# Performance work log

Measured on AMD Instinct MI355X. Metric: run time of the kernel, lower is better.

The kernel has to match this reference:

```python
import jax, jax.numpy as jnp
import numpy as np

B, L, NUM_AA, E, H = 128, 2048, 20, 16, 128

def _mlp(x, W1, b1, W2, b2, W3, b3):
    h = jax.nn.relu(x @ W1 + b1)
    h = jax.nn.relu(h @ W2 + b2)
    return h @ W3 + b3

def _mlp_params(key, in_dim):
    k1, k2, k3 = jax.random.split(key, 3)
    W1 = jax.random.normal(k1, (in_dim, H), jnp.float32) / np.sqrt(in_dim)
    W2 = jax.random.normal(k2, (H, H), jnp.float32) / np.sqrt(H)
    W3 = jax.random.normal(k3, (H, 1), jnp.float32) / np.sqrt(H)
    return W1, jnp.zeros((H,), jnp.float32), W2, jnp.zeros((H,), jnp.float32), W3, jnp.zeros((1,), jnp.float32)

def setup_inputs() -> dict:
    key = jax.random.key(0)
    kR, ks, ke, kl, kt, kp = jax.random.split(key, 6)
    inp = {
        'R': jax.random.normal(kR, (B, L, 3), jnp.float32) * 3.8,  # ~CA-CA scale
        'seq': jax.random.randint(ks, (B, L), 0, NUM_AA),
        'emb': jax.random.normal(ke, (NUM_AA, E), jnp.float32),
    }
    for pref, k, d in (('fl', kl, 1 + 2 * E), ('ft', kt, 1 + 3 * E), ('fp', kp, 2 + 4 * E)):
        W1, b1, W2, b2, W3, b3 = _mlp_params(k, d)
        inp.update({f'{pref}_W1': W1, f'{pref}_b1': b1, f'{pref}_W2': W2, f'{pref}_b2': b2, f'{pref}_W3': W3, f'{pref}_b3': b3})
    return inp

def _energy(R, e, fl, ft, fp):
    d = R[:, 1:, :] - R[:, :-1, :]                      # [B,L-1,3] bond vectors
    lengths = jnp.linalg.norm(d, axis=-1)               # [B,L-1]
    x_l = jnp.concatenate([lengths[..., None], e[:, :-1, :], e[:, 1:, :]], axis=-1)
    E_l = _mlp(x_l, *fl)[..., 0].sum(axis=1)
    # bond angles at atom i+1 between (R[i]-R[i+1]) and (R[i+2]-R[i+1])
    u, v = -d[:, :-1, :], d[:, 1:, :]                   # [B,L-2,3]
    cos_t = jnp.sum(u * v, axis=-1) / (jnp.linalg.norm(u, axis=-1) * jnp.linalg.norm(v, axis=-1))
    theta_in = jnp.clip(cos_t, -1.0, 1.0)               # use_cos_theta=True -> cos(arccos(clip))
    x_t = jnp.concatenate([theta_in[..., None], e[:, :-2, :], e[:, 1:-1, :], e[:, 2:, :]], axis=-1)
    E_t = _mlp(x_t, *ft)[..., 0].sum(axis=1)
    # torsions over quadruples
    b1, b2, b3 = d[:, :-2, :], d[:, 1:-1, :], d[:, 2:, :]
    n1 = jnp.cross(b1, b2)
    n2 = jnp.cross(b2, b3)
    b2u = b2 / jnp.linalg.norm(b2, axis=-1, keepdims=True)
    m1 = jnp.cross(n1, b2u)
    phi = jnp.arctan2(jnp.sum(m1 * n2, axis=-1), jnp.sum(n1 * n2, axis=-1))  # [B,L-3]
    sc = jnp.stack([jnp.sin(phi), jnp.cos(phi)], axis=-1)                    # [B,L-3,2]
    x_p = jnp.concatenate([sc, e[:, :-3, :], e[:, 1:-2, :], e[:, 2:-1, :], e[:, 3:, :]], axis=-1)
    E_p = _mlp(x_p, *fp)[..., 0].sum(axis=1)
    return E_l + E_t + E_p

def reference(R, seq, emb,
              fl_W1, fl_b1, fl_W2, fl_b2, fl_W3, fl_b3,
              ft_W1, ft_b1, ft_W2, ft_b2, ft_W3, ft_b3,
              fp_W1, fp_b1, fp_W2, fp_b2, fp_W3, fp_b3):
    e = emb[seq]                                        # [B,L,E]
    return _energy(R, e,
                   (fl_W1, fl_b1, fl_W2, fl_b2, fl_W3, fl_b3),
                   (ft_W1, ft_b1, ft_W2, ft_b2, ft_W3, ft_b3),
                   (fp_W1, fp_b1, fp_W2, fp_b2, fp_W3, fp_b3))
```

## Files before the change

kernel.cpp:

```cpp
#include <hip/hip_runtime.h>


typedef short bf16x8  __attribute__((ext_vector_type(8)));
typedef float f32x4   __attribute__((ext_vector_type(4)));
typedef float f32x16  __attribute__((ext_vector_type(16)));

constexpr int Lc  = 2048;
constexpr int SHs = 136;

union FragU { uint4 u; bf16x8 v; };

__device__ __forceinline__ unsigned short f2bf(float f) {
    union { float f; unsigned u; } v; v.f = f;
    unsigned u = v.u;
    u = u + 0x7FFFu + ((u >> 16) & 1u);
    return (unsigned short)(u >> 16);
}

__device__ __forceinline__ unsigned pkbf(float a, float b) {
    unsigned ua = __float_as_uint(a) + 0x8000u;
    unsigned ub = __float_as_uint(b) + 0x8000u;
    return __builtin_amdgcn_perm(ub, ua, 0x07060302u);
}

__global__ __launch_bounds__(256)
void prep_kernel(const float* __restrict__ W1_0, const float* __restrict__ b1_0,
                 const float* __restrict__ W1_1, const float* __restrict__ b1_1,
                 const float* __restrict__ W1_2, const float* __restrict__ b1_2,
                 const float* __restrict__ W2_0, const float* __restrict__ W2_1,
                 const float* __restrict__ W2_2,
                 const float* __restrict__ emb, char* __restrict__ ws,
                 float* __restrict__ out)
{
    const int tid = blockIdx.x * 256 + threadIdx.x;
    const int np  = gridDim.x * 256;
    if (blockIdx.x == 0 && threadIdx.x < 128) out[threadIdx.x] = 0.0f;

    unsigned short* d2 = (unsigned short*)ws;
    for (int o = tid; o < 3 * 16384; o += np) {
        int t = o >> 14, r = o & 16383, col = r >> 7, k = r & 127;
        const float* W2 = (t == 0) ? W2_0 : (t == 1) ? W2_1 : W2_2;
        d2[o] = f2bf(W2[k * 128 + col]);
    }
    unsigned short* d1 = (unsigned short*)(ws + 98304);
    for (int o = tid; o < 3 * 12288; o += np) {
        int t = o / 12288, r = o - t * 12288, hid = r / 96, k = r - hid * 96;
        const int NE16 = (t == 0) ? 32 : (t == 1) ? 48 : 64;
        const int NG   = (t == 2) ? 2 : 1;
        const float* W1 = (t == 0) ? W1_0 : (t == 1) ? W1_1 : W1_2;
        const float* b1 = (t == 0) ? b1_0 : (t == 1) ? b1_1 : b1_2;
        float v = 0.0f;
        if (k >= 16) {
            int j = k - 16;
            if (j < NE16) v = W1[(NG + j) * 128 + hid];
        } else if (k == 4) v = b1[hid];
        else if (t == 0 && k == 0) v = W1_0[hid];
        else if (t == 1 && k == 1) v = W1_1[hid];
        else if (t == 2 && k == 2) v = W1_2[hid];
        else if (t == 2 && k == 3) v = W1_2[128 + hid];
        d1[o] = f2bf(v);
    }
    unsigned short* eb = (unsigned short*)(ws + 172032);
    for (int i = tid; i < 320; i += np) eb[i] = f2bf(emb[i]);
}

struct SMem {
    unsigned short H1s[128 * SHs];
    float  Rbuf[393];
    uint2  geomh[128];
    int    seqb[132];
    unsigned short ebuf[320];
    float  part[4];
};

template<int TYPE>
__device__ __forceinline__ void type_pass(
    SMem& sm, const char* __restrict__ ws,
    const float* __restrict__ b2, const float* __restrict__ w3,
    int i0, int wv, int ln31, int hi, f32x4& p4)
{
    constexpr int NEMB  = (TYPE == 0) ? 2 : (TYPE == 1) ? 3 : 4;
    constexpr int STEPS = 1 + NEMB;
    constexpr int ROWSB = Lc - 1 - TYPE;

    const unsigned short* w1t = (const unsigned short*)(ws + 98304 + TYPE * 24576);
    const unsigned short* w2t = (const unsigned short*)(ws + TYPE * 32768);
    const f32x4 z4 = (f32x4){0.f, 0.f, 0.f, 0.f};

    FragU A1[STEPS];
#pragma unroll
    for (int s = 0; s < STEPS; ++s)
        A1[s].u = *(const uint4*)&w1t[(wv * 32 + ln31) * 96 + s * 16 + hi * 8];

#pragma unroll
    for (int h = 0; h < 2; ++h) {
        f32x16 acc1[2];
        acc1[0] = (f32x16)(0.f);
        acc1[1] = (f32x16)(0.f);

#pragma unroll
        for (int s = 0; s < STEPS; ++s) {
#pragma unroll
            for (int rt = 0; rt < 2; ++rt) {
                const int row = h * 64 + rt * 32 + ln31;
                FragU bb;
                if (s == 0) {
                    if (hi == 0) {
                        uint2 g = sm.geomh[row];
                        bb.u = make_uint4(g.x, g.y, 0x00003F80u, 0u);
                    } else {
                        bb.u = make_uint4(0u, 0u, 0u, 0u);
                    }
                } else {
                    bb.u = *(const uint4*)&sm.ebuf[sm.seqb[row + (s - 1)] * 16 + hi * 8];
                }
                acc1[rt] = __builtin_amdgcn_mfma_f32_32x32x16_bf16(A1[s].v, bb.v, acc1[rt], 0, 0, 0);
            }
        }

#pragma unroll
        for (int rt = 0; rt < 2; ++rt) {
            const int row = h * 64 + rt * 32 + ln31;
#pragma unroll
            for (int g = 0; g < 4; ++g) {
                float v0 = fmaxf(acc1[rt][4 * g + 0], 0.f);
                float v1 = fmaxf(acc1[rt][4 * g + 1], 0.f);
                float v2 = fmaxf(acc1[rt][4 * g + 2], 0.f);
                float v3 = fmaxf(acc1[rt][4 * g + 3], 0.f);
                uint2 pk;
                pk.x = pkbf(v0, v1);
                pk.y = pkbf(v2, v3);
                *(uint2*)&sm.H1s[row * SHs + wv * 32 + 8 * g + 4 * hi] = pk;
            }
        }
    }

    FragU B2[8];
#pragma unroll
    for (int s2 = 0; s2 < 8; ++s2)
        B2[s2].u = *(const uint4*)&w2t[(wv * 32 + ln31) * 128 + s2 * 16 + hi * 8];
    const float b2v = b2[wv * 32 + ln31];
    const float w3v = w3[wv * 32 + ln31];
    __syncthreads();

#pragma unroll
    for (int h = 0; h < 2; ++h) {
        f32x16 acc2[2];
        acc2[0] = (f32x16)(0.f);
        acc2[1] = (f32x16)(0.f);
#pragma unroll
        for (int s2 = 0; s2 < 8; ++s2)
#pragma unroll
            for (int rt = 0; rt < 2; ++rt) {
                const int row = h * 64 + rt * 32 + ln31;
                bf16x8 aa = *(const bf16x8*)&sm.H1s[row * SHs + s2 * 16 + hi * 8];
                acc2[rt] = __builtin_amdgcn_mfma_f32_32x32x16_bf16(aa, B2[s2].v, acc2[rt], 0, 0, 0);
            }

#pragma unroll
        for (int rt = 0; rt < 2; ++rt) {
#pragma unroll
            for (int g = 0; g < 4; ++g) {
                const int rbase = i0 + h * 64 + rt * 32 + 8 * g + 4 * hi;
                f32x4 v;
                v[0] = acc2[rt][4 * g + 0]; v[1] = acc2[rt][4 * g + 1];
                v[2] = acc2[rt][4 * g + 2]; v[3] = acc2[rt][4 * g + 3];
                v = __builtin_elementwise_max(v + b2v, z4);
                if (rbase + 3 < ROWSB) {
                    p4 += v * w3v;
                } else {
#pragma unroll
                    for (int rg = 0; rg < 4; ++rg)
                        if (rbase + rg < ROWSB) p4[rg] += v[rg] * w3v;
                }
            }
        }
    }
    __syncthreads();
}

__global__ __launch_bounds__(256, 4)
void energy_kernel(const float* __restrict__ R, const int* __restrict__ seq,
                   const char* __restrict__ ws,
                   const float* b2_0, const float* b2_1, const float* b2_2,
                   const float* w3_0, const float* w3_1, const float* w3_2,
                   const float* b3_0, const float* b3_1, const float* b3_2,
                   float* __restrict__ out)
{
    __shared__ SMem sm;
    const int tid = threadIdx.x;
    const int b   = blockIdx.y;
    const int i0  = blockIdx.x * 128;
    const int lane = tid & 63, wv = tid >> 6;
    const int ln31 = lane & 31, hi = lane >> 5;

    for (int t = tid; t < 393; t += 256) {
        int lr = t / 3, comp = t - lr * 3;
        int row = min(i0 + lr, Lc - 1);
        sm.Rbuf[t] = R[((size_t)b * Lc + row) * 3 + comp];
    }
    for (int t = tid; t < 131; t += 256)
        sm.seqb[t] = seq[b * Lc + min(i0 + t, Lc - 1)];
    {
        const uint4* se = (const uint4*)(ws + 172032);
        for (int t = tid; t < 40; t += 256) ((uint4*)sm.ebuf)[t] = se[t];
    }
    __syncthreads();

    if (tid < 128) {
        const float* p0 = &sm.Rbuf[tid * 3];
        float ax = p0[3] - p0[0], ay = p0[4] - p0[1], az = p0[5] - p0[2];
        float bx = p0[6] - p0[3], by = p0[7] - p0[4], bz = p0[8] - p0[5];
        float cx = p0[9] - p0[6], cy = p0[10] - p0[7], cz = p0[11] - p0[8];
        float na2 = ax * ax + ay * ay + az * az;
        float len = sqrtf(na2);
        float nb2 = bx * bx + by * by + bz * bz;
        float duv = -(ax * bx + ay * by + az * bz);
        float cost = fminf(fmaxf(duv / sqrtf(na2 * nb2), -1.0f), 1.0f);
        float n1x = ay * bz - az * by, n1y = az * bx - ax * bz, n1z = ax * by - ay * bx;
        float n2x = by * cz - bz * cy, n2y = bz * cx - bx * cz, n2z = bx * cy - by * cx;
        float binv = 1.0f / sqrtf(nb2);
        float ux = bx * binv, uy = by * binv, uz = bz * binv;
        float m1x = n1y * uz - n1z * uy, m1y = n1z * ux - n1x * uz, m1z = n1x * uy - n1y * ux;
        float yv = m1x * n2x + m1y * n2y + m1z * n2z;
        float xv = n1x * n2x + n1y * n2y + n1z * n2z;
        float inv = 1.0f / sqrtf(xv * xv + yv * yv);
        sm.geomh[tid] = make_uint2(pkbf(len, cost), pkbf(yv * inv, xv * inv));
    }
    __syncthreads();

    f32x4 p4 = (f32x4){0.f, 0.f, 0.f, 0.f};
    type_pass<0>(sm, ws, b2_0, w3_0, i0, wv, ln31, hi, p4);
    type_pass<1>(sm, ws, b2_1, w3_1, i0, wv, ln31, hi, p4);
    type_pass<2>(sm, ws, b2_2, w3_2, i0, wv, ln31, hi, p4);

    float p = p4[0] + p4[1] + p4[2] + p4[3];
#pragma unroll
    for (int off = 32; off > 0; off >>= 1)
        p += __shfl_down(p, off);
    if (lane == 0) sm.part[wv] = p;
    __syncthreads();
    if (tid == 0) {
        float tot = sm.part[0] + sm.part[1] + sm.part[2] + sm.part[3];
        tot += b3_0[0] * (float)min(Lc - 1 - i0, 128);
        tot += b3_1[0] * (float)min(Lc - 2 - i0, 128);
        tot += b3_2[0] * (float)min(Lc - 3 - i0, 128);
        atomicAdd(&out[b], tot);
    }
}

extern "C" void kernel_launch(void* const* d_in, const int* in_sizes, int n_in,
                              void* d_out, int out_size, void* d_ws, size_t ws_size,
                              hipStream_t stream) {
    const float* R   = (const float*)d_in[0];
    const int*   seq = (const int*)d_in[1];
    const float* emb = (const float*)d_in[2];
    float* out = (float*)d_out;
    char*  ws  = (char*)d_ws;

    prep_kernel<<<dim3(96), dim3(256), 0, stream>>>(
        (const float*)d_in[3],  (const float*)d_in[4],
        (const float*)d_in[9],  (const float*)d_in[10],
        (const float*)d_in[15], (const float*)d_in[16],
        (const float*)d_in[5],  (const float*)d_in[11], (const float*)d_in[17],
        emb, ws, out);

    dim3 grid(16, 128), block(256);
    energy_kernel<<<grid, block, 0, stream>>>(
        R, seq, ws,
        (const float*)d_in[6],  (const float*)d_in[12], (const float*)d_in[18],
        (const float*)d_in[7],  (const float*)d_in[13], (const float*)d_in[19],
        (const float*)d_in[8],  (const float*)d_in[14], (const float*)d_in[20],
        out);
}
```

Before: 150.7 us.

## Keep hidden activations in registers via permlane32 swap instead of LDS round-trip

Restructures each MLP pass so that every wave owns 32 rows and all 128 hidden units. Layer-1 outputs are repacked in registers with v_permlane32_swap into layer-2 A-operand fragments, which removes the H1 shared-memory buffer and the __syncthreads barriers. Weights are relaid in the prep kernel into a fragment-friendly interleaved layout and now stream from global/L2 per MFMA instead of staying resident. Launch bounds drop from 4 to 3 waves per SIMD to make room for the larger accumulators, which risks lower occupancy and more weight-load traffic.

```diff
diff --git a/kernel.cpp b/kernel.cpp
--- a/kernel.cpp
+++ b/kernel.cpp
@@ -5,8 +5,7 @@
 typedef float f32x4   __attribute__((ext_vector_type(4)));
 typedef float f32x16  __attribute__((ext_vector_type(16)));
 
-constexpr int Lc  = 2048;
-constexpr int SHs = 136;
+constexpr int Lc = 2048;
 
 union FragU { uint4 u; bf16x8 v; };
 
@@ -21,6 +20,15 @@
     unsigned ua = __float_as_uint(a) + 0x8000u;
     unsigned ub = __float_as_uint(b) + 0x8000u;
     return __builtin_amdgcn_perm(ub, ua, 0x07060302u);
+}
+
+__device__ __forceinline__ void pl32swap(unsigned &a, unsigned &b) {
+#if __has_builtin(__builtin_amdgcn_permlane32_swap)
+    auto r = __builtin_amdgcn_permlane32_swap(a, b, false, false);
+    a = r[0]; b = r[1];
+#else
+    asm("v_permlane32_swap_b32 %0, %1" : "+v"(a), "+v"(b));
+#endif
 }
 
 __global__ __launch_bounds__(256)
@@ -38,13 +46,17 @@
 
     unsigned short* d2 = (unsigned short*)ws;
     for (int o = tid; o < 3 * 16384; o += np) {
-        int t = o >> 14, r = o & 16383, col = r >> 7, k = r & 127;
+        int t = o >> 14, r = o & 16383;
+        int col = (r >> 3) & 127;
+        int k   = ((r >> 10) << 3) | (r & 7);
         const float* W2 = (t == 0) ? W2_0 : (t == 1) ? W2_1 : W2_2;
         d2[o] = f2bf(W2[k * 128 + col]);
     }
     unsigned short* d1 = (unsigned short*)(ws + 98304);
     for (int o = tid; o < 3 * 12288; o += np) {
-        int t = o / 12288, r = o - t * 12288, hid = r / 96, k = r - hid * 96;
+        int t = o / 12288, r = o - t * 12288;
+        int hid = (r >> 3) & 127;
+        int k   = ((r >> 10) << 3) | (r & 7);
         const int NE16 = (t == 0) ? 32 : (t == 1) ? 48 : 64;
         const int NG   = (t == 2) ? 2 : 1;
         const float* W1 = (t == 0) ? W1_0 : (t == 1) ? W1_1 : W1_2;
@@ -65,17 +77,16 @@
 }
 
 struct SMem {
-    unsigned short H1s[128 * SHs];
     float  Rbuf[393];
     uint2  geomh[128];
     int    seqb[132];
-    unsigned short ebuf[320];
+    alignas(16) unsigned short ebuf[320];
     float  part[4];
 };
 
 template<int TYPE>
 __device__ __forceinline__ void type_pass(
-    SMem& sm, const char* __restrict__ ws,
+    const SMem& sm, const char* __restrict__ ws,
     const float* __restrict__ b2, const float* __restrict__ w3,
     int i0, int wv, int ln31, int hi, f32x4& p4)
 {
@@ -85,101 +96,96 @@
 
     const unsigned short* w1t = (const unsigned short*)(ws + 98304 + TYPE * 24576);
     const unsigned short* w2t = (const unsigned short*)(ws + TYPE * 32768);
+    const int rloc = wv * 32 + ln31;
+
+    f32x16 acc1[4];
+    acc1[0] = (f32x16)(0.f); acc1[1] = (f32x16)(0.f);
+    acc1[2] = (f32x16)(0.f); acc1[3] = (f32x16)(0.f);
+
+#pragma unroll
+    for (int s = 0; s < STEPS; ++s) {
+        FragU bb;
+        if (s == 0) {
+            if (hi == 0) {
+                uint2 g = sm.geomh[rloc];
+                bb.u = make_uint4(g.x, g.y, 0x00003F80u, 0u);
+            } else {
+                bb.u = make_uint4(0u, 0u, 0u, 0u);
+            }
+        } else {
+            bb.u = *(const uint4*)&sm.ebuf[sm.seqb[rloc + (s - 1)] * 16 + hi * 8];
+        }
+#pragma unroll
+        for (int mt = 0; mt < 4; ++mt) {
+            FragU A1;
+            A1.u = *(const uint4*)&w1t[(((s * 2 + hi) * 128) + mt * 32 + ln31) * 8];
+            acc1[mt] = __builtin_amdgcn_mfma_f32_32x32x16_bf16(A1.v, bb.v, acc1[mt], 0, 0, 0);
+        }
+    }
+
+    FragU a2[8];
+#pragma unroll
+    for (int mt = 0; mt < 4; ++mt) {
+        unsigned P0[4], P1[4];
+#pragma unroll
+        for (int g = 0; g < 4; ++g) {
+            float v0 = fmaxf(acc1[mt][4 * g + 0], 0.f);
+            float v1 = fmaxf(acc1[mt][4 * g + 1], 0.f);
+            float v2 = fmaxf(acc1[mt][4 * g + 2], 0.f);
+            float v3 = fmaxf(acc1[mt][4 * g + 3], 0.f);
+            P0[g] = pkbf(v0, v1);
+            P1[g] = pkbf(v2, v3);
+        }
+        unsigned a0 = P0[0], b0 = P0[1]; pl32swap(a0, b0);
+        unsigned a1 = P1[0], b1 = P1[1]; pl32swap(a1, b1);
+        a2[2 * mt].u     = make_uint4(a0, a1, b0, b1);
+        unsigned c0 = P0[2], d0 = P0[3]; pl32swap(c0, d0);
+        unsigned c1 = P1[2], d1 = P1[3]; pl32swap(c1, d1);
+        a2[2 * mt + 1].u = make_uint4(c0, c1, d0, d1);
+    }
+
+    float b2v[4], w3v[4];
+#pragma unroll
+    for (int nt = 0; nt < 4; ++nt) {
+        b2v[nt] = b2[nt * 32 + ln31];
+        w3v[nt] = w3[nt * 32 + ln31];
+    }
+
+    f32x16 acc2[4];
+    acc2[0] = (f32x16)(0.f); acc2[1] = (f32x16)(0.f);
+    acc2[2] = (f32x16)(0.f); acc2[3] = (f32x16)(0.f);
+#pragma unroll
+    for (int s2 = 0; s2 < 8; ++s2) {
+#pragma unroll
+        for (int nt = 0; nt < 4; ++nt) {
+            FragU B2;
+            B2.u = *(const uint4*)&w2t[(((s2 * 2 + hi) * 128) + nt * 32 + ln31) * 8];
+            acc2[nt] = __builtin_amdgcn_mfma_f32_32x32x16_bf16(a2[s2].v, B2.v, acc2[nt], 0, 0, 0);
+        }
+    }
+
     const f32x4 z4 = (f32x4){0.f, 0.f, 0.f, 0.f};
-
-    FragU A1[STEPS];
-#pragma unroll
-    for (int s = 0; s < STEPS; ++s)
-        A1[s].u = *(const uint4*)&w1t[(wv * 32 + ln31) * 96 + s * 16 + hi * 8];
-
-#pragma unroll
-    for (int h = 0; h < 2; ++h) {
-        f32x16 acc1[2];
-        acc1[0] = (f32x16)(0.f);
-        acc1[1] = (f32x16)(0.f);
-
-#pragma unroll
-        for (int s = 0; s < STEPS; ++s) {
-#pragma unroll
-            for (int rt = 0; rt < 2; ++rt) {
-                const int row = h * 64 + rt * 32 + ln31;
-                FragU bb;
-                if (s == 0) {
-                    if (hi == 0) {
-                        uint2 g = sm.geomh[row];
-                        bb.u = make_uint4(g.x, g.y, 0x00003F80u, 0u);
-                    } else {
-                        bb.u = make_uint4(0u, 0u, 0u, 0u);
-                    }
-                } else {
-                    bb.u = *(const uint4*)&sm.ebuf[sm.seqb[row + (s - 1)] * 16 + hi * 8];
-                }
-                acc1[rt] = __builtin_amdgcn_mfma_f32_32x32x16_bf16(A1[s].v, bb.v, acc1[rt], 0, 0, 0);
+#pragma unroll
+    for (int g = 0; g < 4; ++g) {
+        const int rbase = i0 + wv * 32 + 8 * g + 4 * hi;
+#pragma unroll
+        for (int nt = 0; nt < 4; ++nt) {
+            f32x4 v;
+            v[0] = acc2[nt][4 * g + 0]; v[1] = acc2[nt][4 * g + 1];
+            v[2] = acc2[nt][4 * g + 2]; v[3] = acc2[nt][4 * g + 3];
+            v = __builtin_elementwise_max(v + b2v[nt], z4);
+            if (rbase + 3 < ROWSB) {
+                p4 += v * w3v[nt];
+            } else {
+#pragma unroll
+                for (int j = 0; j < 4; ++j)
+                    if (rbase + j < ROWSB) p4[j] += v[j] * w3v[nt];
             }
         }
-
-#pragma unroll
-        for (int rt = 0; rt < 2; ++rt) {
-            const int row = h * 64 + rt * 32 + ln31;
-#pragma unroll
-            for (int g = 0; g < 4; ++g) {
-                float v0 = fmaxf(acc1[rt][4 * g + 0], 0.f);
-                float v1 = fmaxf(acc1[rt][4 * g + 1], 0.f);
-                float v2 = fmaxf(acc1[rt][4 * g + 2], 0.f);
-                float v3 = fmaxf(acc1[rt][4 * g + 3], 0.f);
-                uint2 pk;
-                pk.x = pkbf(v0, v1);
-                pk.y = pkbf(v2, v3);
-                *(uint2*)&sm.H1s[row * SHs + wv * 32 + 8 * g + 4 * hi] = pk;
-            }
-        }
-    }
-
-    FragU B2[8];
-#pragma unroll
-    for (int s2 = 0; s2 < 8; ++s2)
-        B2[s2].u = *(const uint4*)&w2t[(wv * 32 + ln31) * 128 + s2 * 16 + hi * 8];
-    const float b2v = b2[wv * 32 + ln31];
-    const float w3v = w3[wv * 32 + ln31];
-    __syncthreads();
-
-#pragma unroll
-    for (int h = 0; h < 2; ++h) {
-        f32x16 acc2[2];
-        acc2[0] = (f32x16)(0.f);
-        acc2[1] = (f32x16)(0.f);
-#pragma unroll
-        for (int s2 = 0; s2 < 8; ++s2)
-#pragma unroll
-            for (int rt = 0; rt < 2; ++rt) {
-                const int row = h * 64 + rt * 32 + ln31;
-                bf16x8 aa = *(const bf16x8*)&sm.H1s[row * SHs + s2 * 16 + hi * 8];
-                acc2[rt] = __builtin_amdgcn_mfma_f32_32x32x16_bf16(aa, B2[s2].v, acc2[rt], 0, 0, 0);
-            }
-
-#pragma unroll
-        for (int rt = 0; rt < 2; ++rt) {
-#pragma unroll
-            for (int g = 0; g < 4; ++g) {
-                const int rbase = i0 + h * 64 + rt * 32 + 8 * g + 4 * hi;
-                f32x4 v;
-                v[0] = acc2[rt][4 * g + 0]; v[1] = acc2[rt][4 * g + 1];
-                v[2] = acc2[rt][4 * g + 2]; v[3] = acc2[rt][4 * g + 3];
-                v = __builtin_elementwise_max(v + b2v, z4);
-                if (rbase + 3 < ROWSB) {
-                    p4 += v * w3v;
-                } else {
-#pragma unroll
-                    for (int rg = 0; rg < 4; ++rg)
-                        if (rbase + rg < ROWSB) p4[rg] += v[rg] * w3v;
-                }
-            }
-        }
-    }
-    __syncthreads();
-}
-
-__global__ __launch_bounds__(256, 4)
+    }
+}
+
+__global__ __launch_bounds__(256, 3)
 void energy_kernel(const float* __restrict__ R, const int* __restrict__ seq,
                    const char* __restrict__ ws,
                    const float* b2_0, const float* b2_1, const float* b2_2,
```

Measured after the change: 176.4 us. +17.1%, slower.
